# Kernel optimization log

Hardware: AMD Instinct MI355X
Metric: run time of the kernel (lower is better)

## Reference

```python
import jax, jax.numpy as jnp
import numpy as np

C = 256
R = 16  # reduction
CR = C // R
LN_EPS = 1e-5


def setup_inputs() -> dict:
    key = jax.random.key(0)
    ks = jax.random.split(key, 8)
    B, H, W = 16, 128, 128
    x = jax.random.normal(ks[0], (B, C, H, W), dtype=jnp.float32)
    # conv_mask: Conv2d(C, 1, 1x1)
    w_mask = jax.random.normal(ks[1], (C,), dtype=jnp.float32) * (1.0 / np.sqrt(C))
    b_mask = jnp.zeros((), dtype=jnp.float32)
    # channel_add[0]: Conv2d(C, C//R, 1x1)
    w1 = jax.random.normal(ks[2], (CR, C), dtype=jnp.float32) * (1.0 / np.sqrt(C))
    b1 = jnp.zeros((CR,), dtype=jnp.float32)
    # channel_add[1]: LayerNorm([C//R, 1, 1])
    ln_g = jnp.ones((CR,), dtype=jnp.float32)
    ln_b = jnp.zeros((CR,), dtype=jnp.float32)
    # channel_add[3]: Conv2d(C//R, C, 1x1)
    w2 = jax.random.normal(ks[3], (C, CR), dtype=jnp.float32) * (1.0 / np.sqrt(CR))
    b2 = jnp.zeros((C,), dtype=jnp.float32)
    return {"x": x, "w_mask": w_mask, "b_mask": b_mask,
            "w1": w1, "b1": b1, "ln_g": ln_g, "ln_b": ln_b,
            "w2": w2, "b2": b2}


def reference(x, w_mask, b_mask, w1, b1, ln_g, ln_b, w2, b2):
    B, Cc, H, W = x.shape
    # 1x1 conv to 1 channel -> attention logits over H*W
    logits = jnp.einsum('bchw,c->bhw', x, w_mask) + b_mask          # [B,H,W]
    attn = jax.nn.softmax(logits.reshape(B, H * W), axis=-1)        # [B,HW]
    # attention-pooled global context: [B,C]
    context = jnp.einsum('bchw,bs->bc', x, attn.reshape(B, H, W).reshape(B, H * W)[:, :].reshape(B, H * W)) if False else jnp.einsum('bcs,bs->bc', x.reshape(B, Cc, H * W), attn)
    # channel_add MLP: conv1x1 -> LayerNorm over [C//R] -> ReLU -> conv1x1
    t = jnp.einsum('oc,bc->bo', w1, context) + b1                   # [B,C//R]
    mu = jnp.mean(t, axis=-1, keepdims=True)
    var = jnp.mean((t - mu) ** 2, axis=-1, keepdims=True)
    t = (t - mu) / jnp.sqrt(var + LN_EPS) * ln_g + ln_b
    t = jax.nn.relu(t)
    add = jnp.einsum('oc,bc->bo', w2, t) + b2                       # [B,C]
    return x + add[:, :, None, None]
```

## Files before the change

kernel.cpp:

```cpp
#include <hip/hip_runtime.h>
#include <math.h>

#define CC   256
#define CR   16
#define SB   16384
#define NB   16
#define ST   64
#define NT   (SB/ST)
#define LN_EPS 1e-5f

typedef float vfloat4 __attribute__((ext_vector_type(4)));

__global__ __launch_bounds__(256) void k_ctx_partial(const float* __restrict__ x,
                                                     const float* __restrict__ w_mask,
                                                     float* __restrict__ pc,
                                                     float* __restrict__ pm,
                                                     float* __restrict__ ps) {
    __shared__ float tile[CC * ST];
    __shared__ float plog[64 * 17];
    __shared__ float pl[ST];
    __shared__ float wm[CC];

    const int t   = threadIdx.x;
    const int bid = blockIdx.x;
    const int b   = bid / NT;
    const int s0  = (bid % NT) * ST;

    wm[t] = w_mask[t];
    __syncthreads();

    {
        const int c0 = t >> 4;
        const int s4 = (t & 15) << 2;
        const float* xb = x + ((size_t)b * CC) * SB + s0 + s4;
        float4 acc = make_float4(0.f, 0.f, 0.f, 0.f);
#pragma unroll
        for (int k = 0; k < 16; ++k) {
            const int c = c0 + (k << 4);
            const float4 v = *reinterpret_cast<const float4*>(xb + (size_t)c * SB);
            *reinterpret_cast<float4*>(&tile[c * ST + s4]) = v;
            const float w = wm[c];
            acc.x += v.x * w; acc.y += v.y * w; acc.z += v.z * w; acc.w += v.w * w;
        }
        plog[(s4 + 0) * 17 + c0] = acc.x;
        plog[(s4 + 1) * 17 + c0] = acc.y;
        plog[(s4 + 2) * 17 + c0] = acc.z;
        plog[(s4 + 3) * 17 + c0] = acc.w;
    }
    __syncthreads();

    if (t < 64) {
        const int s = t;
        float logit = 0.f;
#pragma unroll
        for (int i = 0; i < 16; ++i) logit += plog[s * 17 + i];
        float m = logit;
#pragma unroll
        for (int off = 32; off > 0; off >>= 1)
            m = fmaxf(m, __shfl_xor(m, off));
        const float p = __expf(logit - m);
        pl[s] = p;
        float sum = p;
#pragma unroll
        for (int off = 32; off > 0; off >>= 1)
            sum += __shfl_xor(sum, off);
        if (s == 0) { pm[bid] = m; ps[bid] = sum; }
    }
    __syncthreads();

    {
        float acc = 0.f;
        const int base = t * ST;
#pragma unroll 8
        for (int j = 0; j < ST; ++j) {
            const int idx = (j + t) & 63;
            acc += tile[base + idx] * pl[idx];
        }
        pc[(size_t)bid * CC + t] = acc;
    }
}

__global__ __launch_bounds__(256) void k_combine_mlp(const float* __restrict__ pc,
                                                     const float* __restrict__ pm,
                                                     const float* __restrict__ ps,
                                                     const float* __restrict__ w1,
                                                     const float* __restrict__ b1,
                                                     const float* __restrict__ ln_g,
                                                     const float* __restrict__ ln_b,
                                                     const float* __restrict__ w2,
                                                     const float* __restrict__ b2,
                                                     float* __restrict__ add) {
    const int b = blockIdx.x;
    const int t = threadIdx.x;
    __shared__ float red[256];
    __shared__ float fx[NT];
    __shared__ float ctx[CC];
    __shared__ float tbuf[CR];
    __shared__ float tn[CR];

    const float m_t = pm[b * NT + t];
    red[t] = m_t; __syncthreads();
    for (int st = 128; st > 0; st >>= 1) {
        if (t < st) red[t] = fmaxf(red[t], red[t + st]);
        __syncthreads();
    }
    const float M = red[0]; __syncthreads();

    const float f = __expf(m_t - M);
    fx[t] = f;
    red[t] = ps[b * NT + t] * f; __syncthreads();
    for (int st = 128; st > 0; st >>= 1) {
        if (t < st) red[t] += red[t + st];
        __syncthreads();
    }
    const float invZ = 1.0f / red[0]; __syncthreads();

    float acc = 0.f;
#pragma unroll 4
    for (int j = 0; j < NT; ++j)
        acc += pc[((size_t)b * NT + j) * CC + t] * fx[j];
    ctx[t] = acc * invZ;
    __syncthreads();

    if (t < CR) {
        float a = b1[t];
        const float* w1r = w1 + (size_t)t * CC;
#pragma unroll 8
        for (int c = 0; c < CC; ++c) a += w1r[c] * ctx[c];
        tbuf[t] = a;
    }
    __syncthreads();
    if (t == 0) {
        float mu = 0.f;
        for (int i = 0; i < CR; ++i) mu += tbuf[i];
        mu *= (1.0f / CR);
        float var = 0.f;
        for (int i = 0; i < CR; ++i) { const float d = tbuf[i] - mu; var += d * d; }
        var *= (1.0f / CR);
        const float inv = rsqrtf(var + LN_EPS);
        for (int i = 0; i < CR; ++i) {
            const float v = (tbuf[i] - mu) * inv * ln_g[i] + ln_b[i];
            tn[i] = v > 0.f ? v : 0.f;
        }
    }
    __syncthreads();

    float a = b2[t];
    const float* w2r = w2 + (size_t)t * CR;
#pragma unroll
    for (int o = 0; o < CR; ++o) a += w2r[o] * tn[o];
    add[(size_t)b * CC + t] = a;
}

__global__ __launch_bounds__(256) void k_add(const float* __restrict__ x,
                                             const float* __restrict__ add,
                                             float* __restrict__ out) {
    const size_t idx = ((size_t)blockIdx.x * 256 + threadIdx.x) * 8;
    const size_t bc = idx / SB;
    const float a = add[bc];
    const float4 v0 = *reinterpret_cast<const float4*>(x + idx);
    const float4 v1 = *reinterpret_cast<const float4*>(x + idx + 4);
    vfloat4 o0 = {v0.x + a, v0.y + a, v0.z + a, v0.w + a};
    vfloat4 o1 = {v1.x + a, v1.y + a, v1.z + a, v1.w + a};
    __builtin_nontemporal_store(o0, reinterpret_cast<vfloat4*>(out + idx));
    __builtin_nontemporal_store(o1, reinterpret_cast<vfloat4*>(out + idx + 4));
}

extern "C" void kernel_launch(void* const* d_in, const int* in_sizes, int n_in,
                              void* d_out, int out_size, void* d_ws, size_t ws_size,
                              hipStream_t stream) {
    const float* x      = (const float*)d_in[0];
    const float* w_mask = (const float*)d_in[1];
    const float* w1     = (const float*)d_in[3];
    const float* b1     = (const float*)d_in[4];
    const float* ln_g   = (const float*)d_in[5];
    const float* ln_b   = (const float*)d_in[6];
    const float* w2     = (const float*)d_in[7];
    const float* b2     = (const float*)d_in[8];
    float* out = (float*)d_out;

    float* ws  = (float*)d_ws;
    float* pc  = ws;
    float* pm  = pc + (size_t)NB * NT * CC;
    float* ps  = pm + (size_t)NB * NT;
    float* add = ps + (size_t)NB * NT;

    k_ctx_partial<<<dim3(NB * NT), dim3(256), 0, stream>>>(x, w_mask, pc, pm, ps);
    k_combine_mlp<<<dim3(NB), dim3(256), 0, stream>>>(pc, pm, ps, w1, b1, ln_g, ln_b, w2, b2, add);
    k_add<<<dim3(NB * CC * SB / 2048), dim3(256), 0, stream>>>(x, add, out);
}
```

Baseline: 173.2 us.

## Widen context-pooling kernel to 1024 threads with wave-shuffle logit reduction

Runs the partial-context kernel with 1024 threads per block instead of 256. Each thread now loads 4 channels instead of 16. Partial logits are reduced with cross-lane shuffles inside each wave before going to shared memory. The attention-weighted pooling is split into four quarter-sums per channel and combined through a shared buffer. The goal is more waves in flight per CU to hide memory latency on the 64 KB LDS tile load, at the cost of an extra shared reduction and a larger block that limits co-resident blocks.

Measured after the change: 176.7 us. Within noise of the previous version (+2.0%).

```diff
diff --git a/kernel.cpp b/kernel.cpp
--- a/kernel.cpp
+++ b/kernel.cpp
@@ -11,22 +11,23 @@
 
 typedef float vfloat4 __attribute__((ext_vector_type(4)));
 
-__global__ __launch_bounds__(256) void k_ctx_partial(const float* __restrict__ x,
-                                                     const float* __restrict__ w_mask,
-                                                     float* __restrict__ pc,
-                                                     float* __restrict__ pm,
-                                                     float* __restrict__ ps) {
+__global__ __launch_bounds__(1024) void k_ctx_partial(const float* __restrict__ x,
+                                                      const float* __restrict__ w_mask,
+                                                      float* __restrict__ pc,
+                                                      float* __restrict__ pm,
+                                                      float* __restrict__ ps) {
     __shared__ float tile[CC * ST];
-    __shared__ float plog[64 * 17];
+    __shared__ float plog[ST * 17];
     __shared__ float pl[ST];
     __shared__ float wm[CC];
+    __shared__ float red2[4 * 260];
 
     const int t   = threadIdx.x;
     const int bid = blockIdx.x;
     const int b   = bid / NT;
     const int s0  = (bid % NT) * ST;
 
-    wm[t] = w_mask[t];
+    if (t < CC) wm[t] = w_mask[t];
     __syncthreads();
 
     {
@@ -35,49 +36,60 @@
         const float* xb = x + ((size_t)b * CC) * SB + s0 + s4;
         float4 acc = make_float4(0.f, 0.f, 0.f, 0.f);
 #pragma unroll
-        for (int k = 0; k < 16; ++k) {
-            const int c = c0 + (k << 4);
+        for (int k = 0; k < 4; ++k) {
+            const int c = c0 + (k << 6);
             const float4 v = *reinterpret_cast<const float4*>(xb + (size_t)c * SB);
             *reinterpret_cast<float4*>(&tile[c * ST + s4]) = v;
             const float w = wm[c];
             acc.x += v.x * w; acc.y += v.y * w; acc.z += v.z * w; acc.w += v.w * w;
         }
-        plog[(s4 + 0) * 17 + c0] = acc.x;
-        plog[(s4 + 1) * 17 + c0] = acc.y;
-        plog[(s4 + 2) * 17 + c0] = acc.z;
-        plog[(s4 + 3) * 17 + c0] = acc.w;
-    }
-    __syncthreads();
-
-    if (t < 64) {
-        const int s = t;
+        acc.x += __shfl_xor(acc.x, 16); acc.y += __shfl_xor(acc.y, 16);
+        acc.z += __shfl_xor(acc.z, 16); acc.w += __shfl_xor(acc.w, 16);
+        acc.x += __shfl_xor(acc.x, 32); acc.y += __shfl_xor(acc.y, 32);
+        acc.z += __shfl_xor(acc.z, 32); acc.w += __shfl_xor(acc.w, 32);
+        const int wv = t >> 6;
+        if ((t & 63) < 16) {
+            plog[(s4 + 0) * 17 + wv] = acc.x;
+            plog[(s4 + 1) * 17 + wv] = acc.y;
+            plog[(s4 + 2) * 17 + wv] = acc.z;
+            plog[(s4 + 3) * 17 + wv] = acc.w;
+        }
+    }
+    __syncthreads();
+
+    if (t < ST) {
         float logit = 0.f;
 #pragma unroll
-        for (int i = 0; i < 16; ++i) logit += plog[s * 17 + i];
+        for (int i = 0; i < 16; ++i) logit += plog[t * 17 + i];
         float m = logit;
 #pragma unroll
         for (int off = 32; off > 0; off >>= 1)
             m = fmaxf(m, __shfl_xor(m, off));
         const float p = __expf(logit - m);
-        pl[s] = p;
+        pl[t] = p;
         float sum = p;
 #pragma unroll
         for (int off = 32; off > 0; off >>= 1)
             sum += __shfl_xor(sum, off);
-        if (s == 0) { pm[bid] = m; ps[bid] = sum; }
+        if (t == 0) { pm[bid] = m; ps[bid] = sum; }
     }
     __syncthreads();
 
     {
-        float acc = 0.f;
-        const int base = t * ST;
-#pragma unroll 8
-        for (int j = 0; j < ST; ++j) {
-            const int idx = (j + t) & 63;
-            acc += tile[base + idx] * pl[idx];
-        }
-        pc[(size_t)bid * CC + t] = acc;
-    }
+        const int c = t >> 2;
+        const int q = t & 3;
+        const int base = c * ST + q * 16;
+        float acc2 = 0.f;
+#pragma unroll
+        for (int j = 0; j < 16; ++j) {
+            const int idx = (j + c) & 15;
+            acc2 += tile[base + idx] * pl[q * 16 + idx];
+        }
+        red2[q * 260 + c] = acc2;
+    }
+    __syncthreads();
+    if (t < CC)
+        pc[(size_t)bid * CC + t] = red2[t] + red2[260 + t] + red2[520 + t] + red2[780 + t];
 }
 
 __global__ __launch_bounds__(256) void k_combine_mlp(const float* __restrict__ pc,
@@ -185,7 +197,7 @@
     float* ps  = pm + (size_t)NB * NT;
     float* add = ps + (size_t)NB * NT;
 
-    k_ctx_partial<<<dim3(NB * NT), dim3(256), 0, stream>>>(x, w_mask, pc, pm, ps);
+    k_ctx_partial<<<dim3(NB * NT), dim3(1024), 0, stream>>>(x, w_mask, pc, pm, ps);
     k_combine_mlp<<<dim3(NB), dim3(256), 0, stream>>>(pc, pm, ps, w1, b1, ln_g, ln_b, w2, b2, add);
     k_add<<<dim3(NB * CC * SB / 2048), dim3(256), 0, stream>>>(x, add, out);
 }
```

## Hold x tile in registers with 1024-thread blocks and wave-shuffle pooling

Applied to the files above, without the earlier changes.

The context kernel now uses 1024-thread blocks covering 256 spatial positions, with each wave owning 16 channels. The x values are kept in registers instead of a 64KB shared-memory tile, and the attention-weighted pooling is done with wave shuffles. This frees LDS and cuts partials from 256 to 64 per batch, which shrinks the combine kernel's work, and that kernel now reduces with a single wave of shuffles. The trade-offs are higher register pressure, more block-level syncs for the max and sum reductions, and only 1024 blocks.

Result: slower. 185.1 us (+6.8%).

```diff
diff --git a/kernel.cpp b/kernel.cpp
--- a/kernel.cpp
+++ b/kernel.cpp
@@ -5,78 +5,82 @@
 #define CR   16
 #define SB   16384
 #define NB   16
-#define ST   64
-#define NT   (SB/ST)
+#define SQ   256
+#define NQ   (SB/SQ)
 #define LN_EPS 1e-5f
 
 typedef float vfloat4 __attribute__((ext_vector_type(4)));
 
-__global__ __launch_bounds__(256) void k_ctx_partial(const float* __restrict__ x,
-                                                     const float* __restrict__ w_mask,
-                                                     float* __restrict__ pc,
-                                                     float* __restrict__ pm,
-                                                     float* __restrict__ ps) {
-    __shared__ float tile[CC * ST];
-    __shared__ float plog[64 * 17];
-    __shared__ float pl[ST];
+__global__ __launch_bounds__(1024) void k_ctx(const float* __restrict__ x,
+                                              const float* __restrict__ w_mask,
+                                              float* __restrict__ pc,
+                                              float* __restrict__ pm,
+                                              float* __restrict__ ps) {
     __shared__ float wm[CC];
+    __shared__ float plog[SQ * 17];
+    __shared__ float red[SQ];
+    __shared__ float pl[SQ];
 
     const int t   = threadIdx.x;
     const int bid = blockIdx.x;
-    const int b   = bid / NT;
-    const int s0  = (bid % NT) * ST;
+    const int b   = bid >> 6;
+    const int sq  = bid & 63;
 
-    wm[t] = w_mask[t];
+    if (t < CC) wm[t] = w_mask[t];
     __syncthreads();
 
-    {
-        const int c0 = t >> 4;
-        const int s4 = (t & 15) << 2;
-        const float* xb = x + ((size_t)b * CC) * SB + s0 + s4;
-        float4 acc = make_float4(0.f, 0.f, 0.f, 0.f);
+    const int w  = t >> 6;
+    const int l  = t & 63;
+    const int s4 = l << 2;
+
+    const float* xb = x + ((size_t)(b * CC + w * 16)) * SB + sq * SQ + s4;
+    vfloat4 v[16];
+    float ax = 0.f, ay = 0.f, az = 0.f, aw = 0.f;
 #pragma unroll
-        for (int k = 0; k < 16; ++k) {
-            const int c = c0 + (k << 4);
-            const float4 v = *reinterpret_cast<const float4*>(xb + (size_t)c * SB);
-            *reinterpret_cast<float4*>(&tile[c * ST + s4]) = v;
-            const float w = wm[c];
-            acc.x += v.x * w; acc.y += v.y * w; acc.z += v.z * w; acc.w += v.w * w;
-        }
-        plog[(s4 + 0) * 17 + c0] = acc.x;
-        plog[(s4 + 1) * 17 + c0] = acc.y;
-        plog[(s4 + 2) * 17 + c0] = acc.z;
-        plog[(s4 + 3) * 17 + c0] = acc.w;
+    for (int k = 0; k < 16; ++k) {
+        v[k] = *reinterpret_cast<const vfloat4*>(xb + (size_t)k * SB);
+        const float wt = wm[w * 16 + k];
+        ax += wt * v[k].x; ay += wt * v[k].y; az += wt * v[k].z; aw += wt * v[k].w;
+    }
+    plog[(s4 + 0) * 17 + w] = ax;
+    plog[(s4 + 1) * 17 + w] = ay;
+    plog[(s4 + 2) * 17 + w] = az;
+    plog[(s4 + 3) * 17 + w] = aw;
+    __syncthreads();
+
+    float logit = 0.f;
+    if (t < SQ) {
+#pragma unroll
+        for (int i = 0; i < 16; ++i) logit += plog[t * 17 + i];
+        red[t] = logit;
     }
     __syncthreads();
+    for (int st = 128; st > 0; st >>= 1) {
+        if (t < st) red[t] = fmaxf(red[t], red[t + st]);
+        __syncthreads();
+    }
+    const float mc = red[0];
+    __syncthreads();
+    if (t < SQ) {
+        const float p = __expf(logit - mc);
+        pl[t] = p; red[t] = p;
+    }
+    __syncthreads();
+    for (int st = 128; st > 0; st >>= 1) {
+        if (t < st) red[t] += red[t + st];
+        __syncthreads();
+    }
+    if (t == 0) { pm[bid] = mc; ps[bid] = red[0]; }
+    __syncthreads();
 
-    if (t < 64) {
-        const int s = t;
-        float logit = 0.f;
+    const vfloat4 p = *reinterpret_cast<const vfloat4*>(&pl[s4]);
 #pragma unroll
-        for (int i = 0; i < 16; ++i) logit += plog[s * 17 + i];
-        float m = logit;
+    for (int k = 0; k < 16; ++k) {
+        float a = v[k].x * p.x + v[k].y * p.y + v[k].z * p.z + v[k].w * p.w;
 #pragma unroll
         for (int off = 32; off > 0; off >>= 1)
-            m = fmaxf(m, __shfl_xor(m, off));
-        const float p = __expf(logit - m);
-        pl[s] = p;
-        float sum = p;
-#pragma unroll
-        for (int off = 32; off > 0; off >>= 1)
-            sum += __shfl_xor(sum, off);
-        if (s == 0) { pm[bid] = m; ps[bid] = sum; }
-    }
-    __syncthreads();
-
-    {
-        float acc = 0.f;
-        const int base = t * ST;
-#pragma unroll 8
-        for (int j = 0; j < ST; ++j) {
-            const int idx = (j + t) & 63;
-            acc += tile[base + idx] * pl[idx];
-        }
-        pc[(size_t)bid * CC + t] = acc;
+            a += __shfl_xor(a, off);
+        if (l == 0) pc[(size_t)bid * CC + w * 16 + k] = a;
     }
 }
 
@@ -92,34 +96,31 @@
                                                      float* __restrict__ add) {
     const int b = blockIdx.x;
     const int t = threadIdx.x;
-    __shared__ float red[256];
-    __shared__ float fx[NT];
+    __shared__ float fxs[NQ];
     __shared__ float ctx[CC];
     __shared__ float tbuf[CR];
     __shared__ float tn[CR];
 
-    const float m_t = pm[b * NT + t];
-    red[t] = m_t; __syncthreads();
-    for (int st = 128; st > 0; st >>= 1) {
-        if (t < st) red[t] = fmaxf(red[t], red[t + st]);
-        __syncthreads();
+    if (t < NQ) {
+        const float m_t = pm[b * NQ + t];
+        float M = m_t;
+#pragma unroll
+        for (int off = 32; off > 0; off >>= 1)
+            M = fmaxf(M, __shfl_xor(M, off));
+        const float f = __expf(m_t - M);
+        float z = ps[b * NQ + t] * f;
+#pragma unroll
+        for (int off = 32; off > 0; off >>= 1)
+            z += __shfl_xor(z, off);
+        fxs[t] = f / z;
     }
-    const float M = red[0]; __syncthreads();
-
-    const float f = __expf(m_t - M);
-    fx[t] = f;
-    red[t] = ps[b * NT + t] * f; __syncthreads();
-    for (int st = 128; st > 0; st >>= 1) {
-        if (t < st) red[t] += red[t + st];
-        __syncthreads();
-    }
-    const float invZ = 1.0f / red[0]; __syncthreads();
+    __syncthreads();
 
     float acc = 0.f;
 #pragma unroll 4
-    for (int j = 0; j < NT; ++j)
-        acc += pc[((size_t)b * NT + j) * CC + t] * fx[j];
-    ctx[t] = acc * invZ;
+    for (int q = 0; q < NQ; ++q)
+        acc += pc[((size_t)b * NQ + q) * CC + t] * fxs[q];
+    ctx[t] = acc;
     __syncthreads();
 
     if (t < CR) {
@@ -132,15 +133,15 @@
     __syncthreads();
     if (t == 0) {
         float mu = 0.f;
-        for (int i = 0; i < CR; ++i) mu += tbuf[i];
+        for (int q = 0; q < CR; ++q) mu += tbuf[q];
         mu *= (1.0f / CR);
         float var = 0.f;
-        for (int i = 0; i < CR; ++i) { const float d = tbuf[i] - mu; var += d * d; }
+        for (int q = 0; q < CR; ++q) { const float d = tbuf[q] - mu; var += d * d; }
         var *= (1.0f / CR);
         const float inv = rsqrtf(var + LN_EPS);
-        for (int i = 0; i < CR; ++i) {
-            const float v = (tbuf[i] - mu) * inv * ln_g[i] + ln_b[i];
-            tn[i] = v > 0.f ? v : 0.f;
+        for (int q = 0; q < CR; ++q) {
+            const float v = (tbuf[q] - mu) * inv * ln_g[q] + ln_b[q];
+            tn[q] = v > 0.f ? v : 0.f;
         }
     }
     __syncthreads();
@@ -181,11 +182,11 @@
 
     float* ws  = (float*)d_ws;
     float* pc  = ws;
-    float* pm  = pc + (size_t)NB * NT * CC;
-    float* ps  = pm + (size_t)NB * NT;
-    float* add = ps + (size_t)NB * NT;
+    float* pm  = pc + (size_t)NB * NQ * CC;
+    float* ps  = pm + (size_t)NB * NQ;
+    float* add = ps + (size_t)NB * NQ;
 
-    k_ctx_partial<<<dim3(NB * NT), dim3(256), 0, stream>>>(x, w_mask, pc, pm, ps);
+    k_ctx<<<dim3(NB * NQ), dim3(1024), 0, stream>>>(x, w_mask, pc, pm, ps);
     k_combine_mlp<<<dim3(NB), dim3(256), 0, stream>>>(pc, pm, ps, w1, b1, ln_g, ln_b, w2, b2, add);
     k_add<<<dim3(NB * CC * SB / 2048), dim3(256), 0, stream>>>(x, add, out);
 }
```
